# Optimization experiments

Hardware: AMD Instinct MI355X
Metric: run time of the kernel (lower is better)

## Reference

```python
import jax, jax.numpy as jnp
import numpy as np

N = 50000
F_IN = 128
HID = 64
HEADS = 4
CLASSES = 16
E = 800000
NEG_SLOPE = 0.2


def _gat_layer(x, src, dst, W, a_src, a_dst, bias, heads, ch, concat):
    n = x.shape[0]
    h = (x @ W).reshape(n, heads, ch)                     # [N,H,C]
    alpha_src = jnp.einsum('nhc,hc->nh', h, a_src)        # [N,H]
    alpha_dst = jnp.einsum('nhc,hc->nh', h, a_dst)        # [N,H]
    e = jax.nn.leaky_relu(alpha_src[src] + alpha_dst[dst], NEG_SLOPE)  # [E,H]
    # segment softmax over edges grouped by destination node
    m = jax.ops.segment_max(e, dst, num_segments=n)       # [N,H]
    ex = jnp.exp(e - m[dst])                              # [E,H]
    s = jax.ops.segment_sum(ex, dst, num_segments=n)      # [N,H]
    alpha = ex / (s[dst] + 1e-16)                         # [E,H]
    # weighted scatter-add aggregation of neighbor features
    out = jax.ops.segment_sum(h[src] * alpha[:, :, None], dst, num_segments=n)  # [N,H,C]
    if concat:
        return out.reshape(n, heads * ch) + bias
    return out.mean(axis=1) + bias


def setup_inputs() -> dict:
    key = jax.random.key(0)
    ks = jax.random.split(key, 12)
    x = jax.random.normal(ks[0], (N, F_IN), dtype=jnp.float32)
    edge_index = jax.random.randint(ks[1], (2, E), 0, N, dtype=jnp.int64)
    g1 = 1.0 / np.sqrt(F_IN)
    g2 = 1.0 / np.sqrt(HID * HEADS)
    W1 = jax.random.normal(ks[2], (F_IN, HEADS * HID), dtype=jnp.float32) * g1
    a_src1 = jax.random.normal(ks[3], (HEADS, HID), dtype=jnp.float32) * g1
    a_dst1 = jax.random.normal(ks[4], (HEADS, HID), dtype=jnp.float32) * g1
    b1 = jnp.zeros((HEADS * HID,), dtype=jnp.float32)
    W2 = jax.random.normal(ks[5], (HEADS * HID, CLASSES), dtype=jnp.float32) * g2
    a_src2 = jax.random.normal(ks[6], (1, CLASSES), dtype=jnp.float32) * g2
    a_dst2 = jax.random.normal(ks[7], (1, CLASSES), dtype=jnp.float32) * g2
    b2 = jnp.zeros((CLASSES,), dtype=jnp.float32)
    return {"x": x, "edge_index": edge_index, "W1": W1, "a_src1": a_src1,
            "a_dst1": a_dst1, "b1": b1, "W2": W2, "a_src2": a_src2,
            "a_dst2": a_dst2, "b2": b2}


def reference(x, edge_index, W1, a_src1, a_dst1, b1, W2, a_src2, a_dst2, b2):
    n = x.shape[0]
    # add self-loops (PyG GATConv default add_self_loops=True)
    loops = jnp.arange(n, dtype=edge_index.dtype)
    src = jnp.concatenate([edge_index[0], loops])
    dst = jnp.concatenate([edge_index[1], loops])
    h = _gat_layer(x, src, dst, W1, a_src1, a_dst1, b1, HEADS, HID, concat=True)
    h = jax.nn.elu(h)
    out = _gat_layer(h, src, dst, W2, a_src2, a_dst2, b2, 1, CLASSES, concat=False)
    return jax.nn.log_softmax(out, axis=1)
```

## Files before the change

### kernel.cpp

```cpp
#include <hip/hip_runtime.h>
#include <hip/hip_fp16.h>
#include <math.h>

#define NEG 0.2f

typedef __attribute__((ext_vector_type(8))) short bf16x8;
typedef __attribute__((ext_vector_type(4))) float f32x4;

__device__ __forceinline__ float lrelu(float x){ return x > 0.f ? x : NEG*x; }

__device__ __forceinline__ float bflo(unsigned u){ return __uint_as_float(u << 16); }
__device__ __forceinline__ float bfhi(unsigned u){ return __uint_as_float(u & 0xffff0000u); }

__device__ __forceinline__ float selh(float a0, float a1, float a2, float a3,
                                      bool bit0, bool bit1){
  float lo = bit0 ? a1 : a0;
  float hi = bit0 ? a3 : a2;
  return bit1 ? hi : lo;
}

__device__ __forceinline__ unsigned short f2bf(float x){
  unsigned u = __float_as_uint(x);
  u += 0x7fffu + ((u >> 16) & 1u);
  return (unsigned short)(u >> 16);
}

#define FMA8(e, h) \
  acc[0]=fmaf(e,bflo(h.x),acc[0]); acc[1]=fmaf(e,bfhi(h.x),acc[1]); \
  acc[2]=fmaf(e,bflo(h.y),acc[2]); acc[3]=fmaf(e,bfhi(h.y),acc[3]); \
  acc[4]=fmaf(e,bflo(h.z),acc[4]); acc[5]=fmaf(e,bfhi(h.z),acc[5]); \
  acc[6]=fmaf(e,bflo(h.w),acc[6]); acc[7]=fmaf(e,bfhi(h.w),acc[7]);

__global__ void fill_kernel(const int* __restrict__ ei,
                            int* __restrict__ cnt, int* __restrict__ adj, int E){
  __shared__ int s_is64;
  if (threadIdx.x < 64){
    int v = ei[2*threadIdx.x + 1];
    unsigned long long b = __ballot(v != 0);
    if (threadIdx.x == 0) s_is64 = (b == 0ULL) ? 1 : 0;
  }
  __syncthreads();
  int is64 = s_is64;
  int stride = gridDim.x * blockDim.x;
  for (int i = blockIdx.x*blockDim.x + threadIdx.x; i < E; i += stride){
    int s = is64 ? ei[2*i]       : ei[i];
    int d = is64 ? ei[2*(E + i)] : ei[E + i];
    int pos = atomicAdd(&cnt[d], 1);
    if (pos < 64) adj[(d << 6) + pos] = s;
  }
}

__device__ __forceinline__ int wt_addr(int col, int k){
  int g = (k >> 3) ^ (col & 7);
  return col*128 + g*8 + (k & 7);
}

__global__ __launch_bounds__(256) void gemm1_mfma(const float* __restrict__ x,
                             const float* __restrict__ W,
                             const float* __restrict__ asrcw, const float* __restrict__ adstw,
                             unsigned short* __restrict__ h1b,
                             float* __restrict__ as1, float* __restrict__ ad1, int N){
  __shared__ unsigned short wt[256*128];
  int t = threadIdx.x;
  int lane = t & 63, w = t >> 6;
  int row0 = blockIdx.x * 64 + w * 16;

  int arow = row0 + (lane & 15);
  if (arow >= N) arow = N - 1;
  const float* xr = x + (size_t)arow * 128 + (lane >> 4) * 8;
  bf16x8 afrag[4];
  #pragma unroll
  for (int kk = 0; kk < 4; kk++){
    float4 p0 = *reinterpret_cast<const float4*>(xr + kk*32);
    float4 p1 = *reinterpret_cast<const float4*>(xr + kk*32 + 4);
    afrag[kk][0] = (short)f2bf(p0.x); afrag[kk][1] = (short)f2bf(p0.y);
    afrag[kk][2] = (short)f2bf(p0.z); afrag[kk][3] = (short)f2bf(p0.w);
    afrag[kk][4] = (short)f2bf(p1.x); afrag[kk][5] = (short)f2bf(p1.y);
    afrag[kk][6] = (short)f2bf(p1.z); afrag[kk][7] = (short)f2bf(p1.w);
  }

  int c = t;
  for (int k0 = 0; k0 < 128; k0 += 8){
    bf16x8 v;
    #pragma unroll
    for (int j = 0; j < 8; j++) v[j] = (short)f2bf(W[(size_t)(k0+j)*256 + c]);
    *reinterpret_cast<bf16x8*>(&wt[wt_addr(c, k0)]) = v;
  }
  __syncthreads();

  f32x4 acc[16];
  #pragma unroll
  for (int n = 0; n < 16; n++) acc[n] = (f32x4){0.f,0.f,0.f,0.f};
  #pragma unroll
  for (int kk = 0; kk < 4; kk++){
    #pragma unroll
    for (int n = 0; n < 16; n++){
      bf16x8 b = *reinterpret_cast<const bf16x8*>(
          &wt[wt_addr(n*16 + (lane & 15), kk*32 + (lane >> 4)*8)]);
      acc[n] = __builtin_amdgcn_mfma_f32_16x16x32_bf16(afrag[kk], b, acc[n], 0, 0, 0);
    }
  }

  int rbase = row0 + (lane >> 4)*4;
  int cbase = lane & 15;
  #pragma unroll
  for (int n = 0; n < 16; n++){
    #pragma unroll
    for (int r = 0; r < 4; r++){
      int row = rbase + r;
      if (row < N) h1b[(size_t)row*256 + n*16 + cbase] = f2bf(acc[n][r]);
    }
  }

  float av[16], dv[16];
  #pragma unroll
  for (int n = 0; n < 16; n++){
    av[n] = asrcw[n*16 + cbase];
    dv[n] = adstw[n*16 + cbase];
  }
  #pragma unroll
  for (int r = 0; r < 4; r++){
    int row = rbase + r;
    float hs[4], hd[4];
    #pragma unroll
    for (int h = 0; h < 4; h++){
      float ps = 0.f, pd = 0.f;
      #pragma unroll
      for (int q = 0; q < 4; q++){
        int n = h*4 + q;
        ps = fmaf(acc[n][r], av[n], ps);
        pd = fmaf(acc[n][r], dv[n], pd);
      }
      #pragma unroll
      for (int off = 1; off < 16; off <<= 1){
        ps += __shfl_xor(ps, off, 64);
        pd += __shfl_xor(pd, off, 64);
      }
      hs[h] = ps; hd[h] = pd;
    }
    if (cbase == 0 && row < N){
      *reinterpret_cast<float4*>(as1 + (size_t)row*4) = make_float4(hs[0],hs[1],hs[2],hs[3]);
      *reinterpret_cast<float4*>(ad1 + (size_t)row*4) = make_float4(hd[0],hd[1],hd[2],hd[3]);
    }
  }
}

__global__ void edge_exp_kernel(const float* __restrict__ as1, const float* __restrict__ ad1,
                                const int* __restrict__ cnt, const int* __restrict__ adj,
                                __half* __restrict__ exarr, float* __restrict__ den, int N){
  int node = (blockIdx.x*blockDim.x + threadIdx.x) >> 6;
  int lane = threadIdx.x & 63;
  if (node >= N) return;
  int cn = cnt[node]; if (cn > 64) cn = 64;
  int beg = node << 6;
  bool val = lane < cn;
  int src = val ? adj[beg + lane] : 0;
  float4 dv = *reinterpret_cast<const float4*>(ad1 + (size_t)node*4);
  float4 sv = *reinterpret_cast<const float4*>(as1 + (size_t)src*4);
  float ex0 = val ? __expf(lrelu(sv.x + dv.x)) : 0.f;
  float ex1 = val ? __expf(lrelu(sv.y + dv.y)) : 0.f;
  float ex2 = val ? __expf(lrelu(sv.z + dv.z)) : 0.f;
  float ex3 = val ? __expf(lrelu(sv.w + dv.w)) : 0.f;

  if (val){
    __half2 p0 = __floats2half2_rn(ex0, ex1);
    __half2 p1 = __floats2half2_rn(ex2, ex3);
    uint2 o;
    o.x = *reinterpret_cast<unsigned*>(&p0);
    o.y = *reinterpret_cast<unsigned*>(&p1);
    *reinterpret_cast<uint2*>(exarr + (size_t)(beg + lane)*4) = o;
  }

  float sp0 = ex0, sp1 = ex1, sp2 = ex2, sp3 = ex3;
  #pragma unroll
  for (int off = 32; off; off >>= 1){
    sp0 += __shfl_xor(sp0, off, 64);
    sp1 += __shfl_xor(sp1, off, 64);
    sp2 += __shfl_xor(sp2, off, 64);
    sp3 += __shfl_xor(sp3, off, 64);
  }
  float4 s2 = *reinterpret_cast<const float4*>(as1 + (size_t)node*4);
  float exs0 = __expf(lrelu(s2.x + dv.x));
  float exs1 = __expf(lrelu(s2.y + dv.y));
  float exs2 = __expf(lrelu(s2.z + dv.z));
  float exs3 = __expf(lrelu(s2.w + dv.w));
  if (lane == 0){
    *reinterpret_cast<float4*>(den + (size_t)node*8) =
        make_float4(sp0 + exs0, sp1 + exs1, sp2 + exs2, sp3 + exs3);
    *reinterpret_cast<float4*>(den + (size_t)node*8 + 4) =
        make_float4(exs0, exs1, exs2, exs3);
  }
}

__global__ void agg1_kernel(const unsigned short* __restrict__ h1b,
                            const float* __restrict__ b1,
                            const int* __restrict__ cnt, const int* __restrict__ adj,
                            const __half* __restrict__ exarr, const float* __restrict__ den,
                            unsigned short* __restrict__ hact_b, int N){
  int wid  = (blockIdx.x*blockDim.x + threadIdx.x) >> 6;
  int lane = threadIdx.x & 63;
  int hf   = lane >> 5;
  int node = (wid << 1) + hf;
  if (node >= N) return;
  int sl = lane & 31;
  int hh = sl >> 3;
  bool hb0 = (sl & 8) != 0, hb1 = (sl & 16) != 0;
  int cn = cnt[node]; if (cn > 64) cn = 64;
  unsigned beg = (unsigned)node << 6;
  const int* aj = adj + beg;
  const __half* exw = exarr + ((size_t)beg * 4);
  unsigned co = (unsigned)sl * 8;

  float acc[8];
  #pragma unroll
  for (int q = 0; q < 8; q++) acc[q] = 0.f;

  int j = 0;
  for (; j + 4 <= cn; j += 4){
    int s0 = aj[j], s1 = aj[j+1], s2 = aj[j+2], s3 = aj[j+3];
    float w0 = __half2float(exw[(unsigned)(j+0)*4 + hh]);
    float w1 = __half2float(exw[(unsigned)(j+1)*4 + hh]);
    float w2 = __half2float(exw[(unsigned)(j+2)*4 + hh]);
    float w3 = __half2float(exw[(unsigned)(j+3)*4 + hh]);
    uint4 h0 = *reinterpret_cast<const uint4*>(h1b + (((unsigned)s0 << 8) + co));
    uint4 h1 = *reinterpret_cast<const uint4*>(h1b + (((unsigned)s1 << 8) + co));
    uint4 h2 = *reinterpret_cast<const uint4*>(h1b + (((unsigned)s2 << 8) + co));
    uint4 h3 = *reinterpret_cast<const uint4*>(h1b + (((unsigned)s3 << 8) + co));
    FMA8(w0, h0); FMA8(w1, h1); FMA8(w2, h2); FMA8(w3, h3);
  }
  for (; j < cn; j++){
    int s0 = aj[j];
    float w0 = __half2float(exw[(unsigned)j*4 + hh]);
    uint4 h0 = *reinterpret_cast<const uint4*>(h1b + (((unsigned)s0 << 8) + co));
    FMA8(w0, h0);
  }

  float4 dn  = *reinterpret_cast<const float4*>(den + (size_t)node*8);
  float4 dsf = *reinterpret_cast<const float4*>(den + (size_t)node*8 + 4);
  float dh  = selh(dn.x, dn.y, dn.z, dn.w, hb0, hb1);
  float ehs = selh(dsf.x, dsf.y, dsf.z, dsf.w, hb0, hb1);
  uint4 hv = *reinterpret_cast<const uint4*>(h1b + (((unsigned)node << 8) + co));
  FMA8(ehs, hv);

  float rinv = 1.0f / (dh + 1e-16f);
  float4 bA = *reinterpret_cast<const float4*>(b1 + co);
  float4 bB = *reinterpret_cast<const float4*>(b1 + co + 4);
  float o[8];
  o[0] = acc[0]*rinv + bA.x; o[1] = acc[1]*rinv + bA.y;
  o[2] = acc[2]*rinv + bA.z; o[3] = acc[3]*rinv + bA.w;
  o[4] = acc[4]*rinv + bB.x; o[5] = acc[5]*rinv + bB.y;
  o[6] = acc[6]*rinv + bB.z; o[7] = acc[7]*rinv + bB.w;
  #pragma unroll
  for (int q = 0; q < 8; q++) o[q] = o[q] > 0.f ? o[q] : (__expf(o[q]) - 1.f);
  uint4 ob;
  ob.x = (unsigned)f2bf(o[0]) | ((unsigned)f2bf(o[1]) << 16);
  ob.y = (unsigned)f2bf(o[2]) | ((unsigned)f2bf(o[3]) << 16);
  ob.z = (unsigned)f2bf(o[4]) | ((unsigned)f2bf(o[5]) << 16);
  ob.w = (unsigned)f2bf(o[6]) | ((unsigned)f2bf(o[7]) << 16);
  *reinterpret_cast<uint4*>(hact_b + (((unsigned)node << 8) + co)) = ob;
}

__device__ __forceinline__ int wt2_addr(int col, int k){
  int g = (k >> 3) ^ (col & 7);
  return col*256 + g*8 + (k & 7);
}

__global__ __launch_bounds__(256) void gemm2_mfma(const unsigned short* __restrict__ hact_b,
                             const float* __restrict__ W2,
                             const float* __restrict__ asrc2, const float* __restrict__ adst2,
                             float* __restrict__ h2, float* __restrict__ as2,
                             float* __restrict__ ad2, int N){
  __shared__ unsigned short wt[16*256];
  int t = threadIdx.x;
  int lane = t & 63, w = t >> 6;
  int row0 = blockIdx.x * 64 + w * 16;

  {
    float4 r0 = *reinterpret_cast<const float4*>(W2 + (size_t)t*16);
    float4 r1 = *reinterpret_cast<const float4*>(W2 + (size_t)t*16 + 4);
    float4 r2 = *reinterpret_cast<const float4*>(W2 + (size_t)t*16 + 8);
    float4 r3 = *reinterpret_cast<const float4*>(W2 + (size_t)t*16 + 12);
    float wr[16] = {r0.x,r0.y,r0.z,r0.w, r1.x,r1.y,r1.z,r1.w,
                    r2.x,r2.y,r2.z,r2.w, r3.x,r3.y,r3.z,r3.w};
    #pragma unroll
    for (int cc = 0; cc < 16; cc++) wt[wt2_addr(cc, t)] = f2bf(wr[cc]);
  }

  int arow = row0 + (lane & 15);
  if (arow >= N) arow = N - 1;
  const unsigned short* hr = hact_b + (size_t)arow*256 + (lane >> 4)*8;
  __syncthreads();

  f32x4 acc = (f32x4){0.f,0.f,0.f,0.f};
  #pragma unroll
  for (int kk = 0; kk < 8; kk++){
    bf16x8 a = *reinterpret_cast<const bf16x8*>(hr + kk*32);
    bf16x8 b = *reinterpret_cast<const bf16x8*>(
        &wt[wt2_addr(lane & 15, kk*32 + (lane >> 4)*8)]);
    acc = __builtin_amdgcn_mfma_f32_16x16x32_bf16(a, b, acc, 0, 0, 0);
  }

  int rbase = row0 + (lane >> 4)*4;
  int cbase = lane & 15;
  float avc = asrc2[cbase], dvc = adst2[cbase];
  #pragma unroll
  for (int r = 0; r < 4; r++){
    int row = rbase + r;
    if (row < N) h2[(size_t)row*16 + cbase] = acc[r];
    float ps = acc[r]*avc, pd = acc[r]*dvc;
    #pragma unroll
    for (int off = 1; off < 16; off <<= 1){
      ps += __shfl_xor(ps, off, 64);
      pd += __shfl_xor(pd, off, 64);
    }
    if (cbase == 0 && row < N){ as2[row] = ps; ad2[row] = pd; }
  }
}

__global__ void agg2_kernel(const float* __restrict__ h2, const float* __restrict__ as2,
                            const float* __restrict__ ad2, const float* __restrict__ b2,
                            const int* __restrict__ cnt, const int* __restrict__ adj,
                            float* __restrict__ out, int N){
  int node = (blockIdx.x*blockDim.x + threadIdx.x) >> 6;
  int lane = threadIdx.x & 63;
  if (node >= N) return;
  int cn = cnt[node]; if (cn > 64) cn = 64;
  int beg = node << 6;
  int g = lane >> 4, c = lane & 15;

  bool val = lane < cn;
  int srcl = val ? adj[beg + lane] : 0;
  float adn = ad2[node];

  float v[16];
  #pragma unroll
  for (int q = 0; q < 16; q++){
    v[q] = 0.f;
    if (4*q < cn){
      int sj = __shfl(srcl, 4*q + g, 64);
      v[q] = h2[((unsigned)sj*16u + (unsigned)c)];
    }
  }

  float e = val ? lrelu(as2[srcl] + adn) : -3e38f;
  float ex = __expf(e);
  float sp = ex;
  #pragma unroll
  for (int off = 32; off; off >>= 1) sp += __shfl_xor(sp, off, 64);
  float eself = __expf(lrelu(as2[node] + adn));
  sp += eself;

  float acc = 0.f;
  #pragma unroll
  for (int q = 0; q < 16; q++){
    if (4*q < cn){
      float wj = __shfl(ex, 4*q + g, 64);
      acc = fmaf(wj, v[q], acc);
    }
  }
  acc += __shfl_xor(acc, 16, 64);
  acc += __shfl_xor(acc, 32, 64);

  if (g == 0){
    acc = fmaf(eself, h2[(size_t)node*16 + c], acc);
    float vv = acc / (sp + 1e-16f) + b2[c];
    float mx = vv;
    #pragma unroll
    for (int off = 1; off < 16; off <<= 1) mx = fmaxf(mx, __shfl_xor(mx, off, 64));
    float se = __expf(vv - mx);
    #pragma unroll
    for (int off = 1; off < 16; off <<= 1) se += __shfl_xor(se, off, 64);
    out[(size_t)node*16 + c] = vv - mx - logf(se);
  }
}

extern "C" void kernel_launch(void* const* d_in, const int* in_sizes, int n_in,
                              void* d_out, int out_size, void* d_ws, size_t ws_size,
                              hipStream_t stream){
  const float* x    = (const float*)d_in[0];
  const int*   ei   = (const int*)d_in[1];
  const float* W1   = (const float*)d_in[2];
  const float* as1w = (const float*)d_in[3];
  const float* ad1w = (const float*)d_in[4];
  const float* b1   = (const float*)d_in[5];
  const float* W2   = (const float*)d_in[6];
  const float* as2w = (const float*)d_in[7];
  const float* ad2w = (const float*)d_in[8];
  const float* b2   = (const float*)d_in[9];
  float* out = (float*)d_out;

  int N = in_sizes[0] / 128;
  int E = in_sizes[1] / 2;

  char* p = (char*)d_ws;
  size_t off = 0;
  auto alloc = [&](size_t b){ size_t c = off; off = (off + b + 255) & ~(size_t)255; return c; };
  unsigned short* h1b   = (unsigned short*)(p + alloc((size_t)N*256*2));
  unsigned short* hact_b= (unsigned short*)(p + alloc((size_t)N*256*2));
  float* h2     = (float*)(p + alloc((size_t)N*16*4));
  float* as1    = (float*)(p + alloc((size_t)N*4*4));
  float* ad1    = (float*)(p + alloc((size_t)N*4*4));
  float* as2    = (float*)(p + alloc((size_t)N*4));
  float* ad2    = (float*)(p + alloc((size_t)N*4));
  int*   cnt    = (int*)(p + alloc((size_t)N*4));
  int*   adj    = (int*)(p + alloc((size_t)N*64*4));
  __half* exarr = (__half*)(p + alloc((size_t)N*64*4*2));
  float* den    = (float*)(p + alloc((size_t)N*8*4));

  hipMemsetAsync(cnt, 0, (size_t)N*4, stream);
  fill_kernel<<<2048, 256, 0, stream>>>(ei, cnt, adj, E);

  gemm1_mfma<<<(N + 63)/64, 256, 0, stream>>>(x, W1, as1w, ad1w, h1b, as1, ad1, N);
  edge_exp_kernel<<<(N*64 + 255)/256, 256, 0, stream>>>(as1, ad1, cnt, adj, exarr, den, N);
  agg1_kernel<<<(((N+1)/2)*64 + 255)/256, 256, 0, stream>>>(h1b, b1, cnt, adj, exarr, den, hact_b, N);
  gemm2_mfma<<<(N + 63)/64, 256, 0, stream>>>(hact_b, W2, as2w, ad2w, h2, as2, ad2, N);
  agg2_kernel<<<(N*64 + 255)/256, 256, 0, stream>>>(h2, as2, ad2, b2, cnt, adj, out, N);
}
```

Before: 188.2 us.

## Fuse edge exponent computation into layer-1 aggregation via shared memory

Removes the separate edge_exp kernel. Each half-wave in agg1 now computes its node's edge attention exponents directly, stores them in fp32 in LDS, and forms the softmax denominator with shuffles. This avoids writing and re-reading the global fp16 exponent array and the denominator buffer, and saves one kernel launch. In exchange, each aggregation wave does extra exp work up front and uses 8 KB of LDS per block, which may reduce occupancy.

```diff
diff --git a/kernel.cpp b/kernel.cpp
--- a/kernel.cpp
+++ b/kernel.cpp
@@ -1,5 +1,4 @@
 #include <hip/hip_runtime.h>
-#include <hip/hip_fp16.h>
 #include <math.h>
 
 #define NEG 0.2f
@@ -145,58 +144,13 @@
   }
 }
 
-__global__ void edge_exp_kernel(const float* __restrict__ as1, const float* __restrict__ ad1,
-                                const int* __restrict__ cnt, const int* __restrict__ adj,
-                                __half* __restrict__ exarr, float* __restrict__ den, int N){
-  int node = (blockIdx.x*blockDim.x + threadIdx.x) >> 6;
-  int lane = threadIdx.x & 63;
-  if (node >= N) return;
-  int cn = cnt[node]; if (cn > 64) cn = 64;
-  int beg = node << 6;
-  bool val = lane < cn;
-  int src = val ? adj[beg + lane] : 0;
-  float4 dv = *reinterpret_cast<const float4*>(ad1 + (size_t)node*4);
-  float4 sv = *reinterpret_cast<const float4*>(as1 + (size_t)src*4);
-  float ex0 = val ? __expf(lrelu(sv.x + dv.x)) : 0.f;
-  float ex1 = val ? __expf(lrelu(sv.y + dv.y)) : 0.f;
-  float ex2 = val ? __expf(lrelu(sv.z + dv.z)) : 0.f;
-  float ex3 = val ? __expf(lrelu(sv.w + dv.w)) : 0.f;
-
-  if (val){
-    __half2 p0 = __floats2half2_rn(ex0, ex1);
-    __half2 p1 = __floats2half2_rn(ex2, ex3);
-    uint2 o;
-    o.x = *reinterpret_cast<unsigned*>(&p0);
-    o.y = *reinterpret_cast<unsigned*>(&p1);
-    *reinterpret_cast<uint2*>(exarr + (size_t)(beg + lane)*4) = o;
-  }
-
-  float sp0 = ex0, sp1 = ex1, sp2 = ex2, sp3 = ex3;
-  #pragma unroll
-  for (int off = 32; off; off >>= 1){
-    sp0 += __shfl_xor(sp0, off, 64);
-    sp1 += __shfl_xor(sp1, off, 64);
-    sp2 += __shfl_xor(sp2, off, 64);
-    sp3 += __shfl_xor(sp3, off, 64);
-  }
-  float4 s2 = *reinterpret_cast<const float4*>(as1 + (size_t)node*4);
-  float exs0 = __expf(lrelu(s2.x + dv.x));
-  float exs1 = __expf(lrelu(s2.y + dv.y));
-  float exs2 = __expf(lrelu(s2.z + dv.z));
-  float exs3 = __expf(lrelu(s2.w + dv.w));
-  if (lane == 0){
-    *reinterpret_cast<float4*>(den + (size_t)node*8) =
-        make_float4(sp0 + exs0, sp1 + exs1, sp2 + exs2, sp3 + exs3);
-    *reinterpret_cast<float4*>(den + (size_t)node*8 + 4) =
-        make_float4(exs0, exs1, exs2, exs3);
-  }
-}
-
-__global__ void agg1_kernel(const unsigned short* __restrict__ h1b,
+__global__ __launch_bounds__(256) void agg1_kernel(
+                            const unsigned short* __restrict__ h1b,
+                            const float* __restrict__ as1, const float* __restrict__ ad1,
                             const float* __restrict__ b1,
                             const int* __restrict__ cnt, const int* __restrict__ adj,
-                            const __half* __restrict__ exarr, const float* __restrict__ den,
                             unsigned short* __restrict__ hact_b, int N){
+  __shared__ float exlds[8][256];
   int wid  = (blockIdx.x*blockDim.x + threadIdx.x) >> 6;
   int lane = threadIdx.x & 63;
   int hf   = lane >> 5;
@@ -208,8 +162,40 @@
   int cn = cnt[node]; if (cn > 64) cn = 64;
   unsigned beg = (unsigned)node << 6;
   const int* aj = adj + beg;
-  const __half* exw = exarr + ((size_t)beg * 4);
   unsigned co = (unsigned)sl * 8;
+  int seg = (((threadIdx.x >> 6) & 3) << 1) + hf;
+  float* exw = &exlds[seg][0];
+
+  float4 dv4 = *reinterpret_cast<const float4*>(ad1 + (size_t)node*4);
+  float4 sv4 = *reinterpret_cast<const float4*>(as1 + (size_t)node*4);
+  float exs[4];
+  exs[0] = __expf(lrelu(sv4.x + dv4.x));
+  exs[1] = __expf(lrelu(sv4.y + dv4.y));
+  exs[2] = __expf(lrelu(sv4.z + dv4.z));
+  exs[3] = __expf(lrelu(sv4.w + dv4.w));
+  float sp[4] = {0.f, 0.f, 0.f, 0.f};
+  #pragma unroll
+  for (int pass = 0; pass < 2; pass++){
+    int s = sl + pass*32;
+    bool val = s < cn;
+    int src = val ? aj[s] : 0;
+    float4 av = *reinterpret_cast<const float4*>(as1 + (size_t)src*4);
+    float e0 = val ? __expf(lrelu(av.x + dv4.x)) : 0.f;
+    float e1 = val ? __expf(lrelu(av.y + dv4.y)) : 0.f;
+    float e2 = val ? __expf(lrelu(av.z + dv4.z)) : 0.f;
+    float e3 = val ? __expf(lrelu(av.w + dv4.w)) : 0.f;
+    *reinterpret_cast<float4*>(&exw[s*4]) = make_float4(e0, e1, e2, e3);
+    sp[0] += e0; sp[1] += e1; sp[2] += e2; sp[3] += e3;
+  }
+  #pragma unroll
+  for (int off = 1; off < 32; off <<= 1){
+    #pragma unroll
+    for (int k = 0; k < 4; k++) sp[k] += __shfl_xor(sp[k], off, 64);
+  }
+  #pragma unroll
+  for (int k = 0; k < 4; k++) sp[k] += exs[k];
+  float dh  = selh(sp[0], sp[1], sp[2], sp[3], hb0, hb1);
+  float ehs = selh(exs[0], exs[1], exs[2], exs[3], hb0, hb1);
 
   float acc[8];
   #pragma unroll
@@ -218,10 +204,10 @@
   int j = 0;
   for (; j + 4 <= cn; j += 4){
     int s0 = aj[j], s1 = aj[j+1], s2 = aj[j+2], s3 = aj[j+3];
-    float w0 = __half2float(exw[(unsigned)(j+0)*4 + hh]);
-    float w1 = __half2float(exw[(unsigned)(j+1)*4 + hh]);
-    float w2 = __half2float(exw[(unsigned)(j+2)*4 + hh]);
-    float w3 = __half2float(exw[(unsigned)(j+3)*4 + hh]);
+    float w0 = exw[(unsigned)(j+0)*4 + hh];
+    float w1 = exw[(unsigned)(j+1)*4 + hh];
+    float w2 = exw[(unsigned)(j+2)*4 + hh];
+    float w3 = exw[(unsigned)(j+3)*4 + hh];
     uint4 h0 = *reinterpret_cast<const uint4*>(h1b + (((unsigned)s0 << 8) + co));
     uint4 h1 = *reinterpret_cast<const uint4*>(h1b + (((unsigned)s1 << 8) + co));
     uint4 h2 = *reinterpret_cast<const uint4*>(h1b + (((unsigned)s2 << 8) + co));
@@ -230,15 +216,11 @@
   }
   for (; j < cn; j++){
     int s0 = aj[j];
-    float w0 = __half2float(exw[(unsigned)j*4 + hh]);
+    float w0 = exw[(unsigned)j*4 + hh];
     uint4 h0 = *reinterpret_cast<const uint4*>(h1b + (((unsigned)s0 << 8) + co));
     FMA8(w0, h0);
   }
 
-  float4 dn  = *reinterpret_cast<const float4*>(den + (size_t)node*8);
-  float4 dsf = *reinterpret_cast<const float4*>(den + (size_t)node*8 + 4);
-  float dh  = selh(dn.x, dn.y, dn.z, dn.w, hb0, hb1);
-  float ehs = selh(dsf.x, dsf.y, dsf.z, dsf.w, hb0, hb1);
   uint4 hv = *reinterpret_cast<const uint4*>(h1b + (((unsigned)node << 8) + co));
   FMA8(ehs, hv);
 
@@ -404,15 +386,12 @@
   float* ad2    = (float*)(p + alloc((size_t)N*4));
   int*   cnt    = (int*)(p + alloc((size_t)N*4));
   int*   adj    = (int*)(p + alloc((size_t)N*64*4));
-  __half* exarr = (__half*)(p + alloc((size_t)N*64*4*2));
-  float* den    = (float*)(p + alloc((size_t)N*8*4));
 
   hipMemsetAsync(cnt, 0, (size_t)N*4, stream);
   fill_kernel<<<2048, 256, 0, stream>>>(ei, cnt, adj, E);
 
   gemm1_mfma<<<(N + 63)/64, 256, 0, stream>>>(x, W1, as1w, ad1w, h1b, as1, ad1, N);
-  edge_exp_kernel<<<(N*64 + 255)/256, 256, 0, stream>>>(as1, ad1, cnt, adj, exarr, den, N);
-  agg1_kernel<<<(((N+1)/2)*64 + 255)/256, 256, 0, stream>>>(h1b, b1, cnt, adj, exarr, den, hact_b, N);
+  agg1_kernel<<<(((N+1)/2)*64 + 255)/256, 256, 0, stream>>>(h1b, as1, ad1, b1, cnt, adj, hact_b, N);
   gemm2_mfma<<<(N + 63)/64, 256, 0, stream>>>(hact_b, W2, as2w, ad2w, h2, as2, ad2, N);
   agg2_kernel<<<(N*64 + 255)/256, 256, 0, stream>>>(h2, as2, ad2, b2, cnt, adj, out, N);
 }
```

Measured after the change: 176.5 us. 1.07x faster.
